# Kernel optimization log

Measured on AMD Instinct MI355X. Metric: run time of the kernel, lower is better.

## Reference

```python
import jax, jax.numpy as jnp
import numpy as np

KERNEL_SIZE = 5


def setup_inputs() -> dict:
    key = jax.random.key(0)
    k1, k2 = jax.random.split(key)
    x = jax.random.normal(k1, (4, 32, 256, 256), dtype=jnp.float32)
    kernel = jax.random.normal(k2, (4, KERNEL_SIZE * KERNEL_SIZE, 256, 256), dtype=jnp.float32)
    return {"x": x, "kernel": kernel}


def reference(x, kernel):
    k = KERNEL_SIZE
    b, kk, h, w = kernel.shape
    # softmax over the k*k dim (original permutes to channels-last then softmax dim=-1)
    kern = jax.nn.softmax(jnp.transpose(kernel, (0, 2, 3, 1)), axis=-1)  # [b,h,w,k*k]
    pad = (k - 1) // 2
    # replicate padding on spatial dims
    xp = jnp.pad(x, ((0, 0), (0, 0), (pad, pad), (pad, pad)), mode="edge")
    # unfold: patch index order is di*k + dj (height offset first), matching torch unfold(2).unfold(3)
    patches = jnp.stack(
        [xp[:, :, i:i + h, j:j + w] for i in range(k) for j in range(k)], axis=-1
    )  # [b,c,h,w,k*k]
    # per-pixel softmax-weighted local sum; kernel broadcast over channel dim
    out = jnp.sum(patches * kern[:, None, :, :, :], axis=-1)  # [b,c,h,w]
    return out
```

## Files before the change

kernel.cpp:

```cpp
#include <hip/hip_runtime.h>

#define HW    256
#define HW2   (HW*HW)
#define KTAPS 25
#define TW    32
#define TH    8
#define LW    36
#define LH    12
#define NEL   (LW*LH)
#define NSTG  7
#define CPB   8
#define C     32

__device__ __forceinline__ void stage_issue(float r[NSTG], const float* __restrict__ xc,
                                            int lane, int h0, int w0) {
#pragma unroll
    for (int k = 0; k < NSTG; ++k) {
        int idx = lane + k * 64;
        if (idx < NEL) {
            int i  = idx / LW;
            int j  = idx - i * LW;
            int hh = min(max(h0 + i - 2, 0), HW - 1);
            int ww = min(max(w0 + j - 2, 0), HW - 1);
            r[k] = xc[hh * HW + ww];
        }
    }
}

__global__ __launch_bounds__(64, 3) void ddown_kernel(
    const float* __restrict__ x,
    const float* __restrict__ kern,
    float* __restrict__ out)
{
    __shared__ __align__(16) float xt[NEL];

    const int lane = threadIdx.x;
    const int txq  = lane & 7;
    const int ty   = lane >> 3;
    const int w0   = blockIdx.x * TW;
    const int h0   = blockIdx.y * TH;
    const int b    = blockIdx.z >> 2;
    const int c0   = (blockIdx.z & 3) * CPB;

    const int h = h0 + ty;
    const int w = w0 + txq * 4;

    const float* xb = x + (size_t)(b * C + c0) * HW2;

    float r[NSTG];
    stage_issue(r, xb, lane, h0, w0);

    const float* kb = kern + (size_t)b * KTAPS * HW2 + h * HW + w;
    float4 wt[KTAPS];
    float sx = 0.f, sy = 0.f, sz = 0.f, sw = 0.f;
#pragma unroll
    for (int j = 0; j < KTAPS; ++j) {
        float4 v = *(const float4*)(kb + (size_t)j * HW2);
        v.x = __expf(v.x); v.y = __expf(v.y); v.z = __expf(v.z); v.w = __expf(v.w);
        sx += v.x; sy += v.y; sz += v.z; sw += v.w;
        wt[j] = v;
    }
    const float ix = 1.f / sx, iy = 1.f / sy, iz = 1.f / sz, iw = 1.f / sw;

    float* ob = out + (size_t)(b * C + c0) * HW2 + h * HW + w;

    for (int cc = 0; cc < CPB; ++cc) {
#pragma unroll
        for (int k = 0; k < NSTG; ++k) {
            int idx = lane + k * 64;
            if (idx < NEL) xt[idx] = r[k];
        }
        if (cc + 1 < CPB) stage_issue(r, xb + (size_t)(cc + 1) * HW2, lane, h0, w0);

        float ax = 0.f, ay = 0.f, az = 0.f, aw = 0.f;
#pragma unroll
        for (int di = 0; di < 5; ++di) {
            const float* row = &xt[(ty + di) * LW + txq * 4];
            float4 pa = *(const float4*)(row);
            float4 pb = *(const float4*)(row + 4);
            float w8[8] = {pa.x, pa.y, pa.z, pa.w, pb.x, pb.y, pb.z, pb.w};
#pragma unroll
            for (int dj = 0; dj < 5; ++dj) {
                float4 wv = wt[di * 5 + dj];
                ax += wv.x * w8[dj + 0];
                ay += wv.y * w8[dj + 1];
                az += wv.z * w8[dj + 2];
                aw += wv.w * w8[dj + 3];
            }
        }
        float4 res = { ax * ix, ay * iy, az * iz, aw * iw };
        *(float4*)(ob + (size_t)cc * HW2) = res;
    }
}

extern "C" void kernel_launch(void* const* d_in, const int* in_sizes, int n_in,
                              void* d_out, int out_size, void* d_ws, size_t ws_size,
                              hipStream_t stream) {
    const float* x    = (const float*)d_in[0];
    const float* kern = (const float*)d_in[1];
    float* out        = (float*)d_out;

    dim3 grid(HW / TW, HW / TH, 4 * 4);
    ddown_kernel<<<grid, 64, 0, stream>>>(x, kern, out);
}
```

Baseline: 109.8 us.

## Stage input tiles asynchronously into a four-deep LDS ring with direct global-to-LDS loads

Result: slower. 151.0 us (+37.5%).

```diff
diff --git a/kernel.cpp b/kernel.cpp
--- a/kernel.cpp
+++ b/kernel.cpp
@@ -9,30 +9,27 @@
 #define LH    12
 #define NEL   (LW*LH)
 #define NSTG  7
+#define BUFSZ (NSTG*64)
+#define NRING 4
 #define CPB   8
 #define C     32
 
-__device__ __forceinline__ void stage_issue(float r[NSTG], const float* __restrict__ xc,
-                                            int lane, int h0, int w0) {
+__device__ __forceinline__ void stage(const float* __restrict__ src, float* dst,
+                                      const int* __restrict__ soff) {
 #pragma unroll
-    for (int k = 0; k < NSTG; ++k) {
-        int idx = lane + k * 64;
-        if (idx < NEL) {
-            int i  = idx / LW;
-            int j  = idx - i * LW;
-            int hh = min(max(h0 + i - 2, 0), HW - 1);
-            int ww = min(max(w0 + j - 2, 0), HW - 1);
-            r[k] = xc[hh * HW + ww];
-        }
-    }
+    for (int k = 0; k < NSTG; ++k)
+        __builtin_amdgcn_global_load_lds(
+            (const __attribute__((address_space(1))) unsigned int*)(src + soff[k]),
+            (__attribute__((address_space(3))) unsigned int*)(dst + k * 64),
+            4, 0, 0);
 }
 
-__global__ __launch_bounds__(64, 3) void ddown_kernel(
+__global__ __launch_bounds__(64, 4) void ddown_kernel(
     const float* __restrict__ x,
     const float* __restrict__ kern,
     float* __restrict__ out)
 {
-    __shared__ __align__(16) float xt[NEL];
+    __shared__ __align__(16) float xt[NRING][BUFSZ];
 
     const int lane = threadIdx.x;
     const int txq  = lane & 7;
@@ -47,8 +44,19 @@
 
     const float* xb = x + (size_t)(b * C + c0) * HW2;
 
-    float r[NSTG];
-    stage_issue(r, xb, lane, h0, w0);
+    int soff[NSTG];
+#pragma unroll
+    for (int k = 0; k < NSTG; ++k) {
+        int idx = lane + k * 64;
+        int i   = idx / LW;
+        int j   = idx - i * LW;
+        int hh  = min(max(h0 + i - 2, 0), HW - 1);
+        int ww  = min(max(w0 + j - 2, 0), HW - 1);
+        soff[k] = hh * HW + ww;
+    }
+
+    stage(xb,       xt[0], soff);
+    stage(xb + HW2, xt[1], soff);
 
     const float* kb = kern + (size_t)b * KTAPS * HW2 + h * HW + w;
     float4 wt[KTAPS];
@@ -64,18 +72,19 @@
 
     float* ob = out + (size_t)(b * C + c0) * HW2 + h * HW + w;
 
+#pragma unroll
     for (int cc = 0; cc < CPB; ++cc) {
-#pragma unroll
-        for (int k = 0; k < NSTG; ++k) {
-            int idx = lane + k * 64;
-            if (idx < NEL) xt[idx] = r[k];
-        }
-        if (cc + 1 < CPB) stage_issue(r, xb + (size_t)(cc + 1) * HW2, lane, h0, w0);
+        if (cc + 2 < CPB) stage(xb + (size_t)(cc + 2) * HW2, xt[(cc + 2) % NRING], soff);
 
+        if (cc < 6)       asm volatile("s_waitcnt vmcnt(14)" ::: "memory");
+        else if (cc == 6) asm volatile("s_waitcnt vmcnt(7)"  ::: "memory");
+        else              asm volatile("s_waitcnt vmcnt(0)"  ::: "memory");
+
+        const float* xc = xt[cc % NRING];
         float ax = 0.f, ay = 0.f, az = 0.f, aw = 0.f;
 #pragma unroll
         for (int di = 0; di < 5; ++di) {
-            const float* row = &xt[(ty + di) * LW + txq * 4];
+            const float* row = &xc[(ty + di) * LW + txq * 4];
             float4 pa = *(const float4*)(row);
             float4 pb = *(const float4*)(row + 4);
             float w8[8] = {pa.x, pa.y, pa.z, pa.w, pb.x, pb.y, pb.z, pb.w};
```
